# Kernel optimization log

Hardware: AMD Instinct MI355X
Metric: run time of the kernel (lower is better)

The kernel has to match this reference:

```python
import jax, jax.numpy as jnp
import numpy as np

HIDDEN = 4096
NH = 32        # query heads
HD = 128       # head dim
NKV = 8        # kv heads
RD = 64        # rotary dim (partial rotary)
THETA = 10000.0
SEQ = 2048


def _rope(x, positions):
    # x: [S, H, HD]; neox-style rope on first RD dims of each head
    half = RD // 2
    inv_freq = 1.0 / (THETA ** (jnp.arange(half, dtype=jnp.float32) / half))
    freqs = positions.astype(jnp.float32)[:, None] * inv_freq[None, :]  # [S, half]
    cos = jnp.cos(freqs)[:, None, :]  # [S,1,half]
    sin = jnp.sin(freqs)[:, None, :]
    x_rot, x_pass = x[..., :RD], x[..., RD:]
    x1, x2 = x_rot[..., :half], x_rot[..., half:]
    o1 = x1 * cos - x2 * sin
    o2 = x2 * cos + x1 * sin
    return jnp.concatenate([o1, o2, x_pass], axis=-1)


def setup_inputs() -> dict:
    key = jax.random.key(0)
    k1, k2, k3 = jax.random.split(key, 3)
    hidden_states = jax.random.normal(k1, (SEQ, HIDDEN), dtype=jnp.float32)
    Wqkv = jax.random.normal(k2, (HIDDEN, (NH + 2 * NKV) * HD), dtype=jnp.float32) * 0.02
    Wo = jax.random.normal(k3, (NH * HD, HIDDEN), dtype=jnp.float32) * 0.02
    positions = jnp.arange(SEQ, dtype=jnp.int64)
    return {"hidden_states": hidden_states, "Wqkv": Wqkv, "Wo": Wo, "positions": positions}


def reference(hidden_states, Wqkv, Wo, positions):
    S = hidden_states.shape[0]
    qkv = hidden_states @ Wqkv  # [S, (NH+2*NKV)*HD]
    q, k, v = jnp.split(qkv, [NH * HD, NH * HD + NKV * HD], axis=-1)
    q = q.reshape(S, NH, HD)
    k = k.reshape(S, NKV, HD)
    v = v.reshape(S, NKV, HD)
    q = _rope(q, positions)
    k = _rope(k, positions)
    # GQA: expand kv heads to query heads
    g = NH // NKV
    k = jnp.repeat(k, g, axis=1)  # [S, NH, HD]
    v = jnp.repeat(v, g, axis=1)
    scale = HD ** -0.5
    scores = jnp.einsum('shd,thd->hst', q, k) * scale  # [NH, S, S]
    causal = jnp.tril(jnp.ones((S, S), dtype=bool))
    scores = jnp.where(causal[None, :, :], scores, jnp.finfo(scores.dtype).min)
    probs = jax.nn.softmax(scores, axis=-1)
    attn = jnp.einsum('hst,thd->shd', probs, v).reshape(S, NH * HD)
    return attn @ Wo
```

## Files before the change

### kernel.cpp

```cpp
#include <hip/hip_runtime.h>

#define S_LEN 2048
#define HID 4096
#define NH 32
#define NKV 8
#define HD 128
#define QKVN 6144
#define KOFF 4096
#define VOFF 5120

typedef unsigned short ushort_t;
typedef unsigned int uint_t;
typedef __attribute__((ext_vector_type(8))) short short8;
typedef __attribute__((ext_vector_type(4))) short short4v;
typedef __attribute__((ext_vector_type(4))) float float4_t;

__device__ __forceinline__ float bf2f(ushort_t u) {
    return __uint_as_float(((uint_t)u) << 16);
}
__device__ __forceinline__ uint_t f2bf(float f) {
    uint_t u = __float_as_uint(f);
    u += 0x7fffu + ((u >> 16) & 1u);
    return u >> 16;
}

__device__ __forceinline__ void gload_lds16(const ushort_t* g, ushort_t* l) {
    __builtin_amdgcn_global_load_lds(
        (const __attribute__((address_space(1))) void*)g,
        (__attribute__((address_space(3))) void*)l, 16, 0, 0);
}

__global__ void f32_to_bf16(const float4* __restrict__ in,
                            short4v* __restrict__ out) {
    int i = blockIdx.x * 256 + threadIdx.x;
    float4 v = in[i];
    short4v o;
    o[0] = (short)f2bf(v.x);
    o[1] = (short)f2bf(v.y);
    o[2] = (short)f2bf(v.z);
    o[3] = (short)f2bf(v.w);
    out[i] = o;
}

__global__ void transpose_f32_bf16(const float* __restrict__ in,
                                   ushort_t* __restrict__ out, int R, int C) {
    __shared__ float t[32][33];
    int c0 = blockIdx.x * 32, r0 = blockIdx.y * 32;
    int ci = threadIdx.x & 31, rb = threadIdx.x >> 5;
#pragma unroll
    for (int p = 0; p < 4; p++) {
        int ri = rb + p * 8;
        t[ri][ci] = in[(size_t)(r0 + ri) * C + c0 + ci];
    }
    __syncthreads();
    int cp = (threadIdx.x & 15) * 2;
    int rw = threadIdx.x >> 4;
#pragma unroll
    for (int p = 0; p < 2; p++) {
        int ri = rw + p * 16;
        uint_t w = f2bf(t[cp][ri]) | (f2bf(t[cp + 1][ri]) << 16);
        *(uint_t*)(&out[(size_t)(c0 + ri) * R + r0 + cp]) = w;
    }
}

__global__ __launch_bounds__(256, 2)
void gemm_bf16(const ushort_t* __restrict__ A, const ushort_t* __restrict__ BT,
               float* __restrict__ Cout, int M, int N, int K) {
    __shared__ __attribute__((aligned(16))) ushort_t As[128 * 32];
    __shared__ __attribute__((aligned(16))) ushort_t Bs[128 * 32];
    const int tid  = threadIdx.x;
    const int wave = tid >> 6;
    const int lane = tid & 63;
    const int quad = lane >> 4;
    const int l16  = lane & 15;
    const int m0 = blockIdx.y * 128;
    const int n0 = blockIdx.x * 128;
    const int wm = (wave & 1) * 64;
    const int wn = (wave >> 1) * 64;

    const int r0 = tid >> 2;
    const int kc = (tid & 3) * 8;
    const ushort_t* gA0 = A  + (size_t)(m0 + r0)      * K + kc;
    const ushort_t* gA1 = A  + (size_t)(m0 + r0 + 64) * K + kc;
    const ushort_t* gB0 = BT + (size_t)(n0 + r0)      * K + kc;
    const ushort_t* gB1 = BT + (size_t)(n0 + r0 + 64) * K + kc;
    ushort_t* lA0 = &As[r0 * 32 + kc];
    ushort_t* lA1 = lA0 + 64 * 32;
    ushort_t* lB0 = &Bs[r0 * 32 + kc];
    ushort_t* lB1 = lB0 + 64 * 32;

    float4_t acc[4][4] = {};

    for (int k0 = 0; k0 < K; k0 += 32) {
        gload_lds16(gA0 + k0, lA0);
        gload_lds16(gA1 + k0, lA1);
        gload_lds16(gB0 + k0, lB0);
        gload_lds16(gB1 + k0, lB1);
        __syncthreads();

        short8 af[4], bfr[4];
#pragma unroll
        for (int i = 0; i < 4; i++)
            af[i] = *(const short8*)(&As[(wm + i * 16 + l16) * 32 + quad * 8]);
#pragma unroll
        for (int j = 0; j < 4; j++)
            bfr[j] = *(const short8*)(&Bs[(wn + j * 16 + l16) * 32 + quad * 8]);
#pragma unroll
        for (int i = 0; i < 4; i++)
#pragma unroll
            for (int j = 0; j < 4; j++)
                acc[i][j] = __builtin_amdgcn_mfma_f32_16x16x32_bf16(
                    af[i], bfr[j], acc[i][j], 0, 0, 0);
        __syncthreads();
    }

#pragma unroll
    for (int i = 0; i < 4; i++)
#pragma unroll
        for (int j = 0; j < 4; j++)
#pragma unroll
            for (int r = 0; r < 4; r++) {
                int row = m0 + wm + i * 16 + quad * 4 + r;
                int col = n0 + wn + j * 16 + l16;
                Cout[(size_t)row * N + col] = acc[i][j][r];
            }
}

__global__ void rope_tab_k(float2* __restrict__ tab) {
    int idx = blockIdx.x * 256 + threadIdx.x;
    int i = idx & 31;
    int s = idx >> 5;
    float invf = exp2f(-(float)i * (13.287712379549449f / 32.0f));
    float fr = (float)s * invf;
    float c, sn;
    sincosf(fr, &sn, &c);
    tab[idx] = make_float2(c, sn);
}

#define QSC 0.12753102543918255f
__global__ void prep_q(const float* __restrict__ qkv, const float2* __restrict__ tab,
                       ushort_t* __restrict__ Qb) {
    int idx = blockIdx.x * 256 + threadIdx.x;
    int d = idx & 127;
    int s = (idx >> 7) & 2047;
    int h = idx >> 18;
    const float* row = qkv + (size_t)s * QKVN + h * HD;
    float v;
    if (d < 64) {
        int i = d & 31;
        float2 cs = tab[(s << 5) + i];
        float x1 = row[i], x2 = row[i + 32];
        v = (d < 32) ? (x1 * cs.x - x2 * cs.y) : (x2 * cs.x + x1 * cs.y);
    } else {
        v = row[d];
    }
    Qb[idx] = (ushort_t)f2bf(v * QSC);
}

__global__ void prep_k(const float* __restrict__ qkv, const float2* __restrict__ tab,
                       ushort_t* __restrict__ Kb) {
    int idx = blockIdx.x * 256 + threadIdx.x;
    int d = idx & 127;
    int t = (idx >> 7) & 2047;
    int hk = idx >> 18;
    const float* row = qkv + (size_t)t * QKVN + KOFF + hk * HD;
    float v;
    if (d < 64) {
        int i = d & 31;
        float2 cs = tab[(t << 5) + i];
        float x1 = row[i], x2 = row[i + 32];
        v = (d < 32) ? (x1 * cs.x - x2 * cs.y) : (x2 * cs.x + x1 * cs.y);
    } else {
        v = row[d];
    }
    Kb[idx] = (ushort_t)f2bf(v);
}

__global__ void prep_v(const float* __restrict__ qkv, ushort_t* __restrict__ Vt) {
    __shared__ float tile[32][33];
    int hk = blockIdx.z;
    int t0 = blockIdx.x * 32, d0 = blockIdx.y * 32;
    int ci = threadIdx.x & 31, rb = threadIdx.x >> 5;
#pragma unroll
    for (int p = 0; p < 4; p++) {
        int tr = rb + p * 8;
        tile[tr][ci] = qkv[(size_t)(t0 + tr) * QKVN + VOFF + hk * HD + d0 + ci];
    }
    __syncthreads();
#pragma unroll
    for (int p = 0; p < 4; p++) {
        int dr = rb + p * 8;
        Vt[((size_t)hk * HD + d0 + dr) * S_LEN + t0 + ci] = (ushort_t)f2bf(tile[ci][dr]);
    }
}

__global__ __launch_bounds__(256, 4)
void flash_attn(const ushort_t* __restrict__ Qb, const ushort_t* __restrict__ Kb,
                const ushort_t* __restrict__ Vt, ushort_t* __restrict__ attn) {
    __shared__ __attribute__((aligned(16))) ushort_t Ks[2][32 * 128];
    __shared__ __attribute__((aligned(16))) ushort_t Vs[2][128 * 32];

    const int h    = blockIdx.y;
    const int hk   = h >> 2;
    const int tid  = threadIdx.x;
    const int wave = tid >> 6;
    const int lane = tid & 63;
    const int quad = lane >> 4;
    const int l16  = lane & 15;
    const int bx   = (int)blockIdx.x;
    const int qt   = bx + 32 * wave;
    const int qw   = qt * 16;

    const ushort_t* Qh = Qb + (size_t)h  * S_LEN * HD;
    const ushort_t* Kh = Kb + (size_t)hk * S_LEN * HD;
    const ushort_t* Vh = Vt + (size_t)hk * HD * S_LEN;

    const int krow = tid >> 4;
    const int ksrc = ((tid & 15) ^ (krow & 7)) << 3;
    const ushort_t* gK0 = Kh + (size_t)krow * HD + ksrc;
    const ushort_t* gK1 = Kh + (size_t)(krow + 16) * HD + ksrc;
    const int vrow = tid >> 2;
    const int vtb  = (tid & 3) << 3;
    const ushort_t* gV0 = Vh + (size_t)vrow * S_LEN + vtb;
    const ushort_t* gV1 = Vh + (size_t)(vrow + 64) * S_LEN + vtb;

    ushort_t* lK = &Ks[0][tid * 8];
    ushort_t* lV = &Vs[0][tid * 8];

#define STAGE(buf, t0)                                                        \
    do {                                                                      \
        gload_lds16(gK0 + (size_t)(t0) * HD, lK + (buf) * (32 * 128));        \
        gload_lds16(gK1 + (size_t)(t0) * HD, lK + (buf) * (32 * 128) + 2048); \
        gload_lds16(gV0 + (t0),              lV + (buf) * (128 * 32));        \
        gload_lds16(gV1 + (t0),              lV + (buf) * (128 * 32) + 2048); \
    } while (0)

    short8 qf[4];
#pragma unroll
    for (int c = 0; c < 4; c++)
        qf[c] = *(const short8*)(Qh + (size_t)(qw + l16) * HD + c * 32 + quad * 8);

    float4_t oacc[8] = {};
    float lsum = 0.f;
    const int s0 = (((quad * 2)     & 3) << 4) | l16;
    const int s1 = (((quad * 2 + 1) & 3) << 4) | l16;

    const int T0w   = qw & ~31;
    const int T0max = ((bx + 96) * 16) & ~31;
    const int kxor  = (l16 & 7) << 3;

    STAGE(0, 0);
    __syncthreads();

#pragma unroll 1
    for (int t0 = 0; t0 <= T0max; t0 += 32) {
        const int cur = (t0 >> 5) & 1;
        if (t0 + 32 <= T0max) STAGE(cur ^ 1, t0 + 32);

        if (t0 <= T0w) {
            const ushort_t* Kbuf = Ks[cur];
            const ushort_t* Vbuf = Vs[cur];

            float4_t stA = {}, stB = {};
#pragma unroll
            for (int c = 0; c < 4; c++) {
                short8 kfA = *(const short8*)(Kbuf + l16 * 128 +
                                              ((c * 32 + quad * 8) ^ kxor));
                short8 kfB = *(const short8*)(Kbuf + (16 + l16) * 128 +
                                              ((c * 32 + quad * 8) ^ kxor));
                stA = __builtin_amdgcn_mfma_f32_16x16x32_bf16(kfA, qf[c], stA, 0, 0, 0);
                stB = __builtin_amdgcn_mfma_f32_16x16x32_bf16(kfB, qf[c], stB, 0, 0, 0);
            }

            const bool maskT = (t0 == T0w);
            float pA[4], pB[4];
#pragma unroll
            for (int r = 0; r < 4; r++) {
                float eA = exp2f(stA[r]);
                float eB = exp2f(stB[r]);
                if (maskT) {
                    int tA = t0 + quad * 4 + r;
                    eA = (tA      <= qw + l16) ? eA : 0.f;
                    eB = (tA + 16 <= qw + l16) ? eB : 0.f;
                }
                pA[r] = eA; pB[r] = eB;
                lsum += eA + eB;
            }

            uint_t a01 = f2bf(pA[0]) | (f2bf(pA[1]) << 16);
            uint_t a23 = f2bf(pA[2]) | (f2bf(pA[3]) << 16);
            uint_t b01 = f2bf(pB[0]) | (f2bf(pB[1]) << 16);
            uint_t b23 = f2bf(pB[2]) | (f2bf(pB[3]) << 16);
            uint_t A01s0 = (uint_t)__shfl((int)a01, s0);
            uint_t A23s0 = (uint_t)__shfl((int)a23, s0);
            uint_t B01s0 = (uint_t)__shfl((int)b01, s0);
            uint_t B23s0 = (uint_t)__shfl((int)b23, s0);
            uint_t A01s1 = (uint_t)__shfl((int)a01, s1);
            uint_t A23s1 = (uint_t)__shfl((int)a23, s1);
            uint_t B01s1 = (uint_t)__shfl((int)b01, s1);
            uint_t B23s1 = (uint_t)__shfl((int)b23, s1);
            uint_t w[4];
            w[0] = quad < 2 ? A01s0 : B01s0;
            w[1] = quad < 2 ? A23s0 : B23s0;
            w[2] = quad < 2 ? A01s1 : B01s1;
            w[3] = quad < 2 ? A23s1 : B23s1;
            short8 pb;
            __builtin_memcpy(&pb, w, 16);

#pragma unroll
            for (int dt = 0; dt < 8; dt++) {
                short8 vf = *(const short8*)(Vbuf + (dt * 16 + l16) * 32 + quad * 8);
                oacc[dt] = __builtin_amdgcn_mfma_f32_16x16x32_bf16(vf, pb, oacc[dt], 0, 0, 0);
            }
        }

        __syncthreads();
    }
#undef STAGE

    lsum += __shfl_xor(lsum, 16);
    lsum += __shfl_xor(lsum, 32);
    float invl = 1.f / lsum;
    ushort_t* orow = attn + (size_t)(qw + l16) * (NH * HD) + h * HD;
#pragma unroll
    for (int dt = 0; dt < 8; dt++) {
        short4v wv;
#pragma unroll
        for (int r = 0; r < 4; r++)
            wv[r] = (short)f2bf(oacc[dt][r] * invl);
        *(short4v*)(orow + dt * 16 + quad * 4) = wv;
    }
}

extern "C" void kernel_launch(void* const* d_in, const int* in_sizes, int n_in,
                              void* d_out, int out_size, void* d_ws, size_t ws_size,
                              hipStream_t stream) {
    const float* hidden = (const float*)d_in[0];
    const float* Wqkv   = (const float*)d_in[1];
    const float* Wo     = (const float*)d_in[2];
    float* out = (float*)d_out;

    char* ws = (char*)d_ws;
    float*    qkv   = (float*)   (ws);
    ushort_t* attnB = (ushort_t*)(ws);
    ushort_t* hidB  = (ushort_t*)(ws + 50331648);
    ushort_t* Qb    = hidB;
    ushort_t* WqkvT = (ushort_t*)(ws + 67108864);
    float2*   rtab  = (float2*)  (ws + 67108864);
    ushort_t* WoT   = (ushort_t*)(ws + 117440512);
    ushort_t* Kb    = (ushort_t*)(ws + 150994944);
    ushort_t* Vt    = (ushort_t*)(ws + 155189248);

    f32_to_bf16<<<(S_LEN * HID) / 1024, 256, 0, stream>>>(
        (const float4*)hidden, (short4v*)hidB);
    transpose_f32_bf16<<<dim3(QKVN / 32, HID / 32), 256, 0, stream>>>(Wqkv, WqkvT, HID, QKVN);
    transpose_f32_bf16<<<dim3(HID / 32, HID / 32), 256, 0, stream>>>(Wo, WoT, HID, HID);

    gemm_bf16<<<dim3(QKVN / 128, S_LEN / 128), 256, 0, stream>>>(
        hidB, WqkvT, qkv, S_LEN, QKVN, HID);

    rope_tab_k<<<(S_LEN * 32) / 256, 256, 0, stream>>>(rtab);
    prep_q<<<(NH  * S_LEN * HD) / 256, 256, 0, stream>>>(qkv, rtab, Qb);
    prep_k<<<(NKV * S_LEN * HD) / 256, 256, 0, stream>>>(qkv, rtab, Kb);
    prep_v<<<dim3(S_LEN / 32, HD / 32, NKV), 256, 0, stream>>>(qkv, Vt);

    flash_attn<<<dim3(32, NH), 256, 0, stream>>>(Qb, Kb, Vt, attnB);

    gemm_bf16<<<dim3(HID / 128, S_LEN / 128), 256, 0, stream>>>(
        attnB, WoT, out, S_LEN, HID, HID);
}
```

Baseline: 561.0 us.

## Process two 16-row query tiles per wave to reuse K/V fragments

Each wave now handles two adjacent 16-row query tiles (even and odd) instead of one. K and V fragments loaded from LDS are reused for both tiles' MFMAs, and the grid is halved to 16 blocks per head. Fewer LDS reads and fewer block-level syncs per unit of work are the goal. The cost is more registers (launch bounds lowered to 3), half as many blocks, and a different causal load balance across waves.

```diff
diff --git a/kernel.cpp b/kernel.cpp
--- a/kernel.cpp
+++ b/kernel.cpp
@@ -194,7 +194,7 @@
     }
 }
 
-__global__ __launch_bounds__(256, 4)
+__global__ __launch_bounds__(256, 3)
 void flash_attn(const ushort_t* __restrict__ Qb, const ushort_t* __restrict__ Kb,
                 const ushort_t* __restrict__ Vt, ushort_t* __restrict__ attn) {
     __shared__ __attribute__((aligned(16))) ushort_t Ks[2][32 * 128];
@@ -208,8 +208,9 @@
     const int quad = lane >> 4;
     const int l16  = lane & 15;
     const int bx   = (int)blockIdx.x;
-    const int qt   = bx + 32 * wave;
-    const int qw   = qt * 16;
+    const int u    = bx + 16 * wave;
+    const int qwE  = u * 32;
+    const int qwO  = qwE + 16;
 
     const ushort_t* Qh = Qb + (size_t)h  * S_LEN * HD;
     const ushort_t* Kh = Kb + (size_t)hk * S_LEN * HD;
@@ -235,18 +236,20 @@
         gload_lds16(gV1 + (t0),              lV + (buf) * (128 * 32) + 2048); \
     } while (0)
 
-    short8 qf[4];
-#pragma unroll
-    for (int c = 0; c < 4; c++)
-        qf[c] = *(const short8*)(Qh + (size_t)(qw + l16) * HD + c * 32 + quad * 8);
-
-    float4_t oacc[8] = {};
-    float lsum = 0.f;
+    short8 qfE[4], qfO[4];
+#pragma unroll
+    for (int c = 0; c < 4; c++) {
+        qfE[c] = *(const short8*)(Qh + (size_t)(qwE + l16) * HD + c * 32 + quad * 8);
+        qfO[c] = *(const short8*)(Qh + (size_t)(qwO + l16) * HD + c * 32 + quad * 8);
+    }
+
+    float4_t oaccE[8] = {}, oaccO[8] = {};
+    float lsumE = 0.f, lsumO = 0.f;
     const int s0 = (((quad * 2)     & 3) << 4) | l16;
     const int s1 = (((quad * 2 + 1) & 3) << 4) | l16;
 
-    const int T0w   = qw & ~31;
-    const int T0max = ((bx + 96) * 16) & ~31;
+    const int T0w   = qwE;
+    const int T0max = (bx + 48) * 32;
     const int kxor  = (l16 & 7) << 3;
 
     STAGE(0, 0);
@@ -261,56 +264,87 @@
             const ushort_t* Kbuf = Ks[cur];
             const ushort_t* Vbuf = Vs[cur];
 
-            float4_t stA = {}, stB = {};
+            float4_t stAE = {}, stBE = {}, stAO = {}, stBO = {};
 #pragma unroll
             for (int c = 0; c < 4; c++) {
                 short8 kfA = *(const short8*)(Kbuf + l16 * 128 +
                                               ((c * 32 + quad * 8) ^ kxor));
                 short8 kfB = *(const short8*)(Kbuf + (16 + l16) * 128 +
                                               ((c * 32 + quad * 8) ^ kxor));
-                stA = __builtin_amdgcn_mfma_f32_16x16x32_bf16(kfA, qf[c], stA, 0, 0, 0);
-                stB = __builtin_amdgcn_mfma_f32_16x16x32_bf16(kfB, qf[c], stB, 0, 0, 0);
+                stAE = __builtin_amdgcn_mfma_f32_16x16x32_bf16(kfA, qfE[c], stAE, 0, 0, 0);
+                stAO = __builtin_amdgcn_mfma_f32_16x16x32_bf16(kfA, qfO[c], stAO, 0, 0, 0);
+                stBE = __builtin_amdgcn_mfma_f32_16x16x32_bf16(kfB, qfE[c], stBE, 0, 0, 0);
+                stBO = __builtin_amdgcn_mfma_f32_16x16x32_bf16(kfB, qfO[c], stBO, 0, 0, 0);
             }
 
             const bool maskT = (t0 == T0w);
-            float pA[4], pB[4];
+            float pAE[4], pBE[4], pAO[4], pBO[4];
 #pragma unroll
             for (int r = 0; r < 4; r++) {
-                float eA = exp2f(stA[r]);
-                float eB = exp2f(stB[r]);
+                float eAE = exp2f(stAE[r]);
+                float eBE = exp2f(stBE[r]);
+                float eAO = exp2f(stAO[r]);
+                float eBO = exp2f(stBO[r]);
                 if (maskT) {
                     int tA = t0 + quad * 4 + r;
-                    eA = (tA      <= qw + l16) ? eA : 0.f;
-                    eB = (tA + 16 <= qw + l16) ? eB : 0.f;
+                    eAE = (tA      <= qwE + l16) ? eAE : 0.f;
+                    eBE = (tA + 16 <= qwE + l16) ? eBE : 0.f;
+                    eAO = (tA      <= qwO + l16) ? eAO : 0.f;
+                    eBO = (tA + 16 <= qwO + l16) ? eBO : 0.f;
                 }
-                pA[r] = eA; pB[r] = eB;
-                lsum += eA + eB;
-            }
-
-            uint_t a01 = f2bf(pA[0]) | (f2bf(pA[1]) << 16);
-            uint_t a23 = f2bf(pA[2]) | (f2bf(pA[3]) << 16);
-            uint_t b01 = f2bf(pB[0]) | (f2bf(pB[1]) << 16);
-            uint_t b23 = f2bf(pB[2]) | (f2bf(pB[3]) << 16);
-            uint_t A01s0 = (uint_t)__shfl((int)a01, s0);
-            uint_t A23s0 = (uint_t)__shfl((int)a23, s0);
-            uint_t B01s0 = (uint_t)__shfl((int)b01, s0);
-            uint_t B23s0 = (uint_t)__shfl((int)b23, s0);
-            uint_t A01s1 = (uint_t)__shfl((int)a01, s1);
-            uint_t A23s1 = (uint_t)__shfl((int)a23, s1);
-            uint_t B01s1 = (uint_t)__shfl((int)b01, s1);
-            uint_t B23s1 = (uint_t)__shfl((int)b23, s1);
-            uint_t w[4];
-            w[0] = quad < 2 ? A01s0 : B01s0;
-            w[1] = quad < 2 ? A23s0 : B23s0;
-            w[2] = quad < 2 ? A01s1 : B01s1;
-            w[3] = quad < 2 ? A23s1 : B23s1;
-            short8 pb;
-            __builtin_memcpy(&pb, w, 16);
+                pAE[r] = eAE; pBE[r] = eBE;
+                pAO[r] = eAO; pBO[r] = eBO;
+                lsumE += eAE + eBE;
+                lsumO += eAO + eBO;
+            }
+
+            short8 pbE, pbO;
+            {
+                uint_t a01 = f2bf(pAE[0]) | (f2bf(pAE[1]) << 16);
+                uint_t a23 = f2bf(pAE[2]) | (f2bf(pAE[3]) << 16);
+                uint_t b01 = f2bf(pBE[0]) | (f2bf(pBE[1]) << 16);
+                uint_t b23 = f2bf(pBE[2]) | (f2bf(pBE[3]) << 16);
+                uint_t A01s0 = (uint_t)__shfl((int)a01, s0);
+                uint_t A23s0 = (uint_t)__shfl((int)a23, s0);
+                uint_t B01s0 = (uint_t)__shfl((int)b01, s0);
+                uint_t B23s0 = (uint_t)__shfl((int)b23, s0);
+                uint_t A01s1 = (uint_t)__shfl((int)a01, s1);
+                uint_t A23s1 = (uint_t)__shfl((int)a23, s1);
+                uint_t B01s1 = (uint_t)__shfl((int)b01, s1);
+                uint_t B23s1 = (uint_t)__shfl((int)b23, s1);
+                uint_t w[4];
+                w[0] = quad < 2 ? A01s0 : B01s0;
+                w[1] = quad < 2 ? A23s0 : B23s0;
+                w[2] = quad < 2 ? A01s1 : B01s1;
+                w[3] = quad < 2 ? A23s1 : B23s1;
+                __builtin_memcpy(&pbE, w, 16);
+            }
+            {
+                uint_t a01 = f2bf(pAO[0]) | (f2bf(pAO[1]) << 16);
+                uint_t a23 = f2bf(pAO[2]) | (f2bf(pAO[3]) << 16);
+                uint_t b01 = f2bf(pBO[0]) | (f2bf(pBO[1]) << 16);
+                uint_t b23 = f2bf(pBO[2]) | (f2bf(pBO[3]) << 16);
+                uint_t A01s0 = (uint_t)__shfl((int)a01, s0);
+                uint_t A23s0 = (uint_t)__shfl((int)a23, s0);
+                uint_t B01s0 = (uint_t)__shfl((int)b01, s0);
+                uint_t B23s0 = (uint_t)__shfl((int)b23, s0);
+                uint_t A01s1 = (uint_t)__shfl((int)a01, s1);
+                uint_t A23s1 = (uint_t)__shfl((int)a23, s1);
+                uint_t B01s1 = (uint_t)__shfl((int)b01, s1);
+                uint_t B23s1 = (uint_t)__shfl((int)b23, s1);
+                uint_t w[4];
+                w[0] = quad < 2 ? A01s0 : B01s0;
+                w[1] = quad < 2 ? A23s0 : B23s0;
+                w[2] = quad < 2 ? A01s1 : B01s1;
+                w[3] = quad < 2 ? A23s1 : B23s1;
+                __builtin_memcpy(&pbO, w, 16);
+            }
 
 #pragma unroll
             for (int dt = 0; dt < 8; dt++) {
                 short8 vf = *(const short8*)(Vbuf + (dt * 16 + l16) * 32 + quad * 8);
-                oacc[dt] = __builtin_amdgcn_mfma_f32_16x16x32_bf16(vf, pb, oacc[dt], 0, 0, 0);
+                oaccE[dt] = __builtin_amdgcn_mfma_f32_16x16x32_bf16(vf, pbE, oaccE[dt], 0, 0, 0);
+                oaccO[dt] = __builtin_amdgcn_mfma_f32_16x16x32_bf16(vf, pbO, oaccO[dt], 0, 0, 0);
             }
         }
 
@@ -318,17 +352,24 @@
     }
 #undef STAGE
 
-    lsum += __shfl_xor(lsum, 16);
-    lsum += __shfl_xor(lsum, 32);
-    float invl = 1.f / lsum;
-    ushort_t* orow = attn + (size_t)(qw + l16) * (NH * HD) + h * HD;
+    lsumE += __shfl_xor(lsumE, 16);
+    lsumE += __shfl_xor(lsumE, 32);
+    lsumO += __shfl_xor(lsumO, 16);
+    lsumO += __shfl_xor(lsumO, 32);
+    float invlE = 1.f / lsumE;
+    float invlO = 1.f / lsumO;
+    ushort_t* orowE = attn + (size_t)(qwE + l16) * (NH * HD) + h * HD;
+    ushort_t* orowO = attn + (size_t)(qwO + l16) * (NH * HD) + h * HD;
 #pragma unroll
     for (int dt = 0; dt < 8; dt++) {
-        short4v wv;
-#pragma unroll
-        for (int r = 0; r < 4; r++)
-            wv[r] = (short)f2bf(oacc[dt][r] * invl);
-        *(short4v*)(orow + dt * 16 + quad * 4) = wv;
+        short4v wvE, wvO;
+#pragma unroll
+        for (int r = 0; r < 4; r++) {
+            wvE[r] = (short)f2bf(oaccE[dt][r] * invlE);
+            wvO[r] = (short)f2bf(oaccO[dt][r] * invlO);
+        }
+        *(short4v*)(orowE + dt * 16 + quad * 4) = wvE;
+        *(short4v*)(orowO + dt * 16 + quad * 4) = wvO;
     }
 }
 
@@ -364,7 +405,7 @@
     prep_k<<<(NKV * S_LEN * HD) / 256, 256, 0, stream>>>(qkv, rtab, Kb);
     prep_v<<<dim3(S_LEN / 32, HD / 32, NKV), 256, 0, stream>>>(qkv, Vt);
 
-    flash_attn<<<dim3(32, NH), 256, 0, stream>>>(Qb, Kb, Vt, attnB);
+    flash_attn<<<dim3(16, NH), 256, 0, stream>>>(Qb, Kb, Vt, attnB);
 
     gemm_bf16<<<dim3(HID / 128, S_LEN / 128), 256, 0, stream>>>(
         attnB, WoT, out, S_LEN, HID, HID);
```

Result: no change. 569.7 us (+1.5%).
